# Kernel optimization log

Measured on AMD Instinct MI355X. Metric: run time of the kernel, lower is better.

Reference implementation:

```python
import jax, jax.numpy as jnp
import numpy as np

D_MODEL = 1024
N_HEADS = 16
D_FF = 4096
D_K = D_MODEL // N_HEADS


def _ln(x, g, b, eps=1e-5):
    mu = jnp.mean(x, axis=-1, keepdims=True)
    var = jnp.mean(jnp.square(x - mu), axis=-1, keepdims=True)
    return (x - mu) * jax.lax.rsqrt(var + eps) * g + b


def setup_inputs() -> dict:
    key = jax.random.key(0)
    ks = jax.random.split(key, 16)
    s = 0.02
    inp = {
        "x": jax.random.normal(ks[0], (2, 2048, D_MODEL), dtype=jnp.float32),
        "Wq": jax.random.normal(ks[1], (D_MODEL, D_MODEL), dtype=jnp.float32) * s,
        "bq": jnp.zeros((D_MODEL,), jnp.float32),
        "Wk": jax.random.normal(ks[2], (D_MODEL, D_MODEL), dtype=jnp.float32) * s,
        "bk": jnp.zeros((D_MODEL,), jnp.float32),
        "Wv": jax.random.normal(ks[3], (D_MODEL, D_MODEL), dtype=jnp.float32) * s,
        "bv": jnp.zeros((D_MODEL,), jnp.float32),
        "Wo": jax.random.normal(ks[4], (D_MODEL, D_MODEL), dtype=jnp.float32) * s,
        "bo": jnp.zeros((D_MODEL,), jnp.float32),
        "W1": jax.random.normal(ks[5], (D_MODEL, D_FF), dtype=jnp.float32) * s,
        "b1": jnp.zeros((D_FF,), jnp.float32),
        "W2": jax.random.normal(ks[6], (D_FF, D_MODEL), dtype=jnp.float32) * s,
        "b2": jnp.zeros((D_MODEL,), jnp.float32),
        "g1": jnp.ones((D_MODEL,), jnp.float32),
        "be1": jnp.zeros((D_MODEL,), jnp.float32),
        "g2": jnp.ones((D_MODEL,), jnp.float32),
        "be2": jnp.zeros((D_MODEL,), jnp.float32),
    }
    return inp


def reference(x, Wq, bq, Wk, bk, Wv, bv, Wo, bo, W1, b1, W2, b2, g1, be1, g2, be2):
    B, L, D = x.shape
    # QKV projections -> [B, H, L, d_k]
    q = (x @ Wq + bq).reshape(B, L, N_HEADS, D_K).transpose(0, 2, 1, 3)
    k = (x @ Wk + bk).reshape(B, L, N_HEADS, D_K).transpose(0, 2, 1, 3)
    v = (x @ Wv + bv).reshape(B, L, N_HEADS, D_K).transpose(0, 2, 1, 3)
    scores = jnp.einsum("bhqd,bhkd->bhqk", q, k) / jnp.sqrt(jnp.float32(D_K))
    attn = jax.nn.softmax(scores, axis=-1)
    ctx = jnp.einsum("bhqk,bhkd->bhqd", attn, v)
    ctx = ctx.transpose(0, 2, 1, 3).reshape(B, L, D)
    attn_out = ctx @ Wo + bo
    # residual + LN1
    h = _ln(x + attn_out, g1, be1)
    # FFN (exact GELU, matching torch F.gelu default)
    ff = jax.nn.gelu(h @ W1 + b1, approximate=False) @ W2 + b2
    return _ln(h + ff, g2, be2)
```

## Files before the change

### kernel.cpp

```cpp
#include <hip/hip_runtime.h>
#include <cmath>


typedef unsigned short u16;
typedef unsigned int u32;
typedef __attribute__((ext_vector_type(8))) __bf16 bf16x8;
typedef __attribute__((ext_vector_type(4))) float f32x4;

#define MFMA16(a, b, c) __builtin_amdgcn_mfma_f32_16x16x32_bf16(a, b, c, 0, 0, 0)

__device__ __forceinline__ u16 f2bf(float f) {
  u32 u = __builtin_bit_cast(u32, f);
  u += 0x7fffu + ((u >> 16) & 1u);
  return (u16)(u >> 16);
}

__device__ __forceinline__ u32 packtrunc(float lo, float hi) {
#if __has_builtin(__builtin_amdgcn_perm)
  return __builtin_amdgcn_perm(__builtin_bit_cast(u32, hi),
                               __builtin_bit_cast(u32, lo), 0x07060302u);
#else
  return (__builtin_bit_cast(u32, lo) >> 16) |
         (__builtin_bit_cast(u32, hi) & 0xFFFF0000u);
#endif
}

__device__ __forceinline__ bf16x8 ld_frag(const u16* p) {
  return __builtin_bit_cast(bf16x8, *(const uint4*)p);
}

__device__ __forceinline__ float fexp2(float x) {
#if __has_builtin(__builtin_amdgcn_exp2f)
  return __builtin_amdgcn_exp2f(x);
#else
  return exp2f(x);
#endif
}

__device__ __forceinline__ void gload16(const u16* g, u16* l) {
  __builtin_amdgcn_global_load_lds(
      (const __attribute__((address_space(1))) void*)g,
      (__attribute__((address_space(3))) void*)l, 16, 0, 0);
}

#define WAITVL(N) asm volatile("s_waitcnt vmcnt(" #N ") lgkmcnt(0)" ::: "memory")
#define BAR() do { __builtin_amdgcn_s_barrier(); asm volatile("" ::: "memory"); } while (0)

__global__ __launch_bounds__(256) void cvt_bf16_k(const float* __restrict__ src,
                                                  u16* __restrict__ dst) {
  int i = (blockIdx.x * 256 + threadIdx.x) * 4;
  float4 v = *(const float4*)(src + i);
  ushort4 o;
  o.x = f2bf(v.x); o.y = f2bf(v.y); o.z = f2bf(v.z); o.w = f2bf(v.w);
  *(ushort4*)(dst + i) = o;
}

__global__ __launch_bounds__(256) void transpose_bf16_k(const float* __restrict__ src,
                                                        u16* __restrict__ dst,
                                                        int R, int C) {
  __shared__ float tile[32][33];
  int tx = threadIdx.x & 31, ty = threadIdx.x >> 5;
  int c0 = blockIdx.x * 32, r0 = blockIdx.y * 32;
#pragma unroll
  for (int i = 0; i < 4; i++)
    tile[ty + 8 * i][tx] = src[(long)(r0 + ty + 8 * i) * C + c0 + tx];
  __syncthreads();
#pragma unroll
  for (int i = 0; i < 4; i++)
    dst[(long)(c0 + ty + 8 * i) * R + r0 + tx] = f2bf(tile[tx][ty + 8 * i]);
}

__global__ __launch_bounds__(256) void transpose4_bf16_k(
    const float* __restrict__ Wq, const float* __restrict__ Wk,
    const float* __restrict__ Wv, const float* __restrict__ Wo,
    u16* __restrict__ wqkvT, u16* __restrict__ woT) {
  const int z = blockIdx.z;
  const float* src = (z == 0) ? Wq : (z == 1) ? Wk : (z == 2) ? Wv : Wo;
  u16* dst = (z < 3) ? (wqkvT + (size_t)z * 1024 * 1024) : woT;
  __shared__ float tile[32][33];
  int tx = threadIdx.x & 31, ty = threadIdx.x >> 5;
  int c0 = blockIdx.x * 32, r0 = blockIdx.y * 32;
#pragma unroll
  for (int i = 0; i < 4; i++)
    tile[ty + 8 * i][tx] = src[(long)(r0 + ty + 8 * i) * 1024 + c0 + tx];
  __syncthreads();
#pragma unroll
  for (int i = 0; i < 4; i++)
    dst[(long)(c0 + ty + 8 * i) * 1024 + r0 + tx] = f2bf(tile[tx][ty + 8 * i]);
}

template <int MODE>
__global__ __launch_bounds__(512, 2) void gemm256_k(
    const u16* __restrict__ A, const u16* __restrict__ BT,
    int N, int lda, int ldb, int Kc,
    const float* __restrict__ bias, float* __restrict__ outF, u16* __restrict__ outB,
    float* __restrict__ p1, float* __restrict__ p2, float* __restrict__ p3,
    u16* __restrict__ qd, u16* __restrict__ kd, u16* __restrict__ vTd,
    const float* __restrict__ bq, const float* __restrict__ bk, const float* __restrict__ bv) {
  __shared__ u16 As[4][256 * 32];
  __shared__ u16 Bs[4][256 * 32];
  const int tid = threadIdx.x;
  const int wave = tid >> 6, lane = tid & 63, quad = lane >> 4, l16 = lane & 15;
  const int wm = wave >> 2, wn = wave & 3;
  const int m0 = blockIdx.y * 256, n0 = blockIdx.x * 256;
  const int kz = blockIdx.z;
  const long kofs = (long)kz * Kc;
  const int KT = Kc >> 5;

  const int srow = lane >> 2;
  const int sseg = (lane & 3) ^ (srow & 3);
  const u16* aS = A + (long)(m0 + wave * 32 + srow) * lda + kofs + sseg * 8;
  const u16* bS = BT + (long)(n0 + wave * 32 + srow) * ldb + kofs + sseg * 8;

  auto stageA = [&](int sb, int s) {
    const u16* p = aS + (long)s * 32;
    gload16(p, &As[sb][wave * 1024]);
    gload16(p + 16 * (long)lda, &As[sb][wave * 1024 + 512]);
  };
  auto stageB = [&](int sb, int s) {
    const u16* p = bS + (long)s * 32;
    gload16(p, &Bs[sb][wave * 1024]);
    gload16(p + 16 * (long)ldb, &Bs[sb][wave * 1024 + 512]);
  };

  int aro[8], bro[4];
#pragma unroll
  for (int mf = 0; mf < 8; mf++) {
    int r = wm * 128 + mf * 16 + l16;
    aro[mf] = r * 32 + ((quad ^ (r & 3)) * 8);
  }
#pragma unroll
  for (int nf = 0; nf < 4; nf++) {
    int r = wn * 64 + nf * 16 + l16;
    bro[nf] = r * 32 + ((quad ^ (r & 3)) * 8);
  }

  f32x4 acc[8][4] = {};

  stageA(0, 0); stageB(0, 0);
  stageA(1, 1); stageB(1, 1);
  stageA(2, 2); stageB(2, 2);

#pragma unroll 1
  for (int t = 0; t < KT; ++t) {
    const int buf = t & 3;
    if (t < KT - 2)      { WAITVL(8); }
    else if (t == KT - 2){ WAITVL(4); }
    else                 { WAITVL(0); }
    BAR();

    bf16x8 af[4], bf4[4];
#pragma unroll
    for (int i = 0; i < 4; i++) af[i] = ld_frag(&As[buf][aro[i]]);
#pragma unroll
    for (int i = 0; i < 4; i++) bf4[i] = ld_frag(&Bs[buf][bro[i]]);
    if (t + 3 < KT) stageA((t + 3) & 3, t + 3);
    BAR();
    __builtin_amdgcn_s_setprio(1);
#pragma unroll
    for (int mf = 0; mf < 4; mf++)
#pragma unroll
      for (int nf = 0; nf < 4; nf++)
        acc[mf][nf] = MFMA16(af[mf], bf4[nf], acc[mf][nf]);
    __builtin_amdgcn_s_setprio(0);

    bf16x8 ag[4];
#pragma unroll
    for (int i = 0; i < 4; i++) ag[i] = ld_frag(&As[buf][aro[4 + i]]);
    if (t + 3 < KT) stageB((t + 3) & 3, t + 3);
    BAR();
    __builtin_amdgcn_s_setprio(1);
#pragma unroll
    for (int mf = 0; mf < 4; mf++)
#pragma unroll
      for (int nf = 0; nf < 4; nf++)
        acc[4 + mf][nf] = MFMA16(ag[mf], bf4[nf], acc[4 + mf][nf]);
    __builtin_amdgcn_s_setprio(0);
  }

  if (MODE == 0) {
    const int nbase = n0 + wn * 64;
    const int mat = nbase >> 10;
    const float* bp = (mat == 0) ? bq : ((mat == 1) ? bk : bv);
    float bb[4];
    int hh0[4], dd0[4];
#pragma unroll
    for (int nf = 0; nf < 4; nf++) {
      int nn = (nbase + nf * 16 + l16) & 1023;
      bb[nf] = bp[nn];
      hh0[nf] = nn >> 6;
      dd0[nf] = nn & 63;
    }
    if (mat < 2) {
#pragma unroll
      for (int mf = 0; mf < 8; mf++) {
#pragma unroll
        for (int r = 0; r < 4; r++) {
          int mr = m0 + wm * 128 + mf * 16 + quad * 4 + r;
          int bI = mr >> 11, ll = mr & 2047;
#pragma unroll
          for (int nf = 0; nf < 4; nf++) {
            float v = acc[mf][nf][r] + bb[nf];
            long idx = ((long)((bI * 16 + hh0[nf]) * 2048 + ll)) * 64 + dd0[nf];
            if (mat == 0) {
              qd[idx] = f2bf(v * 0.18033688011112043f);
            } else {
              kd[idx] = f2bf(v);
            }
          }
        }
      }
    } else {
#pragma unroll
      for (int nf = 0; nf < 4; nf++) {
#pragma unroll
        for (int mf = 0; mf < 8; mf++) {
#pragma unroll
          for (int r = 0; r < 4; r++) {
            int mr = m0 + wm * 128 + mf * 16 + quad * 4 + r;
            int bI = mr >> 11, ll = mr & 2047;
            float v = acc[mf][nf][r] + bb[nf];
            vTd[((long)((bI * 16 + hh0[nf]) * 64 + dd0[nf])) * 2048 + ll] = f2bf(v);
          }
        }
      }
    }
  } else if (MODE == 2) {
    float bb[4];
#pragma unroll
    for (int nf = 0; nf < 4; nf++) bb[nf] = bias[n0 + wn * 64 + nf * 16 + l16];
#pragma unroll
    for (int mf = 0; mf < 8; mf++) {
#pragma unroll
      for (int r = 0; r < 4; r++) {
        int mr = m0 + wm * 128 + mf * 16 + quad * 4 + r;
        u16* orow = outB + (long)mr * N + n0 + wn * 64 + l16;
#pragma unroll
        for (int nf = 0; nf < 4; nf++) {
          float v = acc[mf][nf][r] + bb[nf];
          v = 0.5f * v * (1.0f + erff(v * 0.70710678118654752f));
          orow[nf * 16] = f2bf(v);
        }
      }
    }
  } else {
    float* sl = (kz == 0) ? outF : (kz == 1) ? p1 : (kz == 2) ? p2 : p3;
#pragma unroll
    for (int mf = 0; mf < 8; mf++) {
#pragma unroll
      for (int r = 0; r < 4; r++) {
        int mr = m0 + wm * 128 + mf * 16 + quad * 4 + r;
        float* orow = sl + (long)mr * N + n0 + wn * 64 + l16;
#pragma unroll
        for (int nf = 0; nf < 4; nf++) orow[nf * 16] = acc[mf][nf][r];
      }
    }
  }
}

template <int MODE, int TN>
__global__ __launch_bounds__(256) void gemm_k(
    const u16* __restrict__ A, const u16* __restrict__ BT, int M, int N, int K,
    const float* __restrict__ bias, float* __restrict__ outF, u16* __restrict__ outB,
    u16* __restrict__ qd, u16* __restrict__ kd, u16* __restrict__ vTd,
    const float* __restrict__ bq, const float* __restrict__ bk, const float* __restrict__ bv) {
  constexpr int NT = TN / 32;
  __shared__ u16 As[2][128 * 32];
  __shared__ u16 Bs[2][TN * 32];
  const int tid = threadIdx.x;
  const int wave = tid >> 6, lane = tid & 63, quad = lane >> 4, l16 = lane & 15;
  const int wm = wave >> 1, wn = wave & 1;
  const int m0 = blockIdx.y * 128, n0 = blockIdx.x * TN;

  const int srow = lane >> 2;
  const int sxor = (lane & 3) ^ (srow & 3);
  const u16* aS0 = A + (long)(m0 + wave * 32 + srow) * K + sxor * 8;
  const u16* aS1 = aS0 + 16 * K;
  const u16* bS0 = BT + (long)(n0 + (TN == 128 ? wave * 32 : wave * 16) + srow) * K + sxor * 8;
  const u16* bS1 = bS0 + 16 * K;

  int aoff[4], boff[NT];
#pragma unroll
  for (int t = 0; t < 4; t++) {
    int ra = wm * 64 + t * 16 + l16;
    aoff[t] = ra * 32 + ((quad ^ (l16 & 3)) * 8);
  }
#pragma unroll
  for (int t = 0; t < NT; t++) {
    int rb = wn * (TN / 2) + t * 16 + l16;
    boff[t] = rb * 32 + ((quad ^ (l16 & 3)) * 8);
  }

  auto stage = [&](int buf, int k0) {
    gload16(aS0 + k0, &As[buf][(wave * 2 + 0) * 512]);
    gload16(aS1 + k0, &As[buf][(wave * 2 + 1) * 512]);
    if (TN == 128) {
      gload16(bS0 + k0, &Bs[buf][(wave * 2 + 0) * 512]);
      gload16(bS1 + k0, &Bs[buf][(wave * 2 + 1) * 512]);
    } else {
      gload16(bS0 + k0, &Bs[buf][wave * 512]);
    }
  };

  f32x4 acc[4][NT] = {};

  stage(0, 0);
#pragma unroll 1
  for (int k0 = 0; k0 < K; k0 += 32) {
    const int buf = (k0 >> 5) & 1;
    __syncthreads();
    if (k0 + 32 < K) stage(buf ^ 1, k0 + 32);
    bf16x8 af[4], bfr[NT];
#pragma unroll
    for (int t = 0; t < 4; t++) af[t] = ld_frag(&As[buf][aoff[t]]);
#pragma unroll
    for (int t = 0; t < NT; t++) bfr[t] = ld_frag(&Bs[buf][boff[t]]);
#pragma unroll
    for (int mt = 0; mt < 4; mt++)
#pragma unroll
      for (int nt = 0; nt < NT; nt++)
        acc[mt][nt] = MFMA16(af[mt], bfr[nt], acc[mt][nt]);
  }

  if (MODE == 1) {
    float bb[NT];
#pragma unroll
    for (int nt = 0; nt < NT; nt++) bb[nt] = bias[n0 + wn * (TN / 2) + nt * 16 + l16];
#pragma unroll
    for (int mt = 0; mt < 4; mt++) {
#pragma unroll
      for (int r = 0; r < 4; r++) {
        int mr = m0 + wm * 64 + mt * 16 + quad * 4 + r;
        float* orow = outF + (long)mr * N + n0 + wn * (TN / 2) + l16;
#pragma unroll
        for (int nt = 0; nt < NT; nt++)
          orow[nt * 16] = acc[mt][nt][r] + bb[nt];
      }
    }
  }
}

__global__ __launch_bounds__(256) void attn_k(const u16* __restrict__ qd,
                                              const u16* __restrict__ kd,
                                              const u16* __restrict__ vTd,
                                              float* __restrict__ oP0,
                                              float* __restrict__ oP1,
                                              float* __restrict__ ml0,
                                              float* __restrict__ ml1) {
  __shared__ u16 Ks[2][64 * 64];
  __shared__ u16 Vs[2][64 * 64];
  __shared__ __align__(16) u16 P[4][32][72];
  const int tid = threadIdx.x;
  const int wave = tid >> 6, lane = tid & 63, quad = lane >> 4, l16 = lane & 15;
  const int bh = blockIdx.y;
  const int kz = blockIdx.z;
  const int jbeg = kz * 1024, jend = jbeg + 1024;
  const u16* Q = qd + (long)bh * 2048 * 64;
  const u16* Kp = kd + (long)bh * 2048 * 64;
  const u16* Vt = vTd + (long)bh * 64 * 2048;
  const int qbase = blockIdx.x * 128 + wave * 32;

  bf16x8 qf[2][2];
#pragma unroll
  for (int qs = 0; qs < 2; qs++) {
    qf[qs][0] = ld_frag(Q + (qbase + qs * 16 + l16) * 64 + quad * 8);
    qf[qs][1] = ld_frag(Q + (qbase + qs * 16 + l16) * 64 + 32 + quad * 8);
  }

  f32x4 o[2][4] = {};
  float m[2] = {-1e30f, -1e30f}, l[2] = {0.f, 0.f};

  const int srow = lane >> 3;
  const int sx = (lane & 7) ^ srow;
  const int kr0 = wave * 16 + srow;
  const int kr1 = wave * 16 + 8 + srow;

  const int fs0 = ((0 * 4 + quad) ^ (l16 & 7)) * 8;
  const int fs1 = ((1 * 4 + quad) ^ (l16 & 7)) * 8;

  auto stage = [&](int buf, int j0) {
    gload16(Kp + (long)(j0 + kr0) * 64 + sx * 8, &Ks[buf][(wave * 2 + 0) * 512]);
    gload16(Kp + (long)(j0 + kr1) * 64 + sx * 8, &Ks[buf][(wave * 2 + 1) * 512]);
    gload16(Vt + (long)kr0 * 2048 + j0 + sx * 8, &Vs[buf][(wave * 2 + 0) * 512]);
    gload16(Vt + (long)kr1 * 2048 + j0 + sx * 8, &Vs[buf][(wave * 2 + 1) * 512]);
  };

  stage(0, jbeg);

#pragma unroll 1
  for (int j0 = jbeg; j0 < jend; j0 += 64) {
    const int buf = (j0 >> 6) & 1;
    __syncthreads();
    if (j0 + 64 < jend) stage(buf ^ 1, j0 + 64);

    const u16* kb = &Ks[buf][0];
    f32x4 st[2][4];
#pragma unroll
    for (int f = 0; f < 4; f++) {
      bf16x8 k0 = ld_frag(kb + (f * 16 + l16) * 64 + fs0);
      bf16x8 k1 = ld_frag(kb + (f * 16 + l16) * 64 + fs1);
      f32x4 s0 = {}, s1 = {};
      s0 = MFMA16(k0, qf[0][0], s0); s0 = MFMA16(k1, qf[0][1], s0);
      s1 = MFMA16(k0, qf[1][0], s1); s1 = MFMA16(k1, qf[1][1], s1);
      st[0][f] = s0; st[1][f] = s1;
    }

#pragma unroll
    for (int qs = 0; qs < 2; qs++) {
      float mx = -1e30f;
#pragma unroll
      for (int f = 0; f < 4; f++)
        mx = fmaxf(mx, fmaxf(fmaxf(st[qs][f][0], st[qs][f][1]),
                             fmaxf(st[qs][f][2], st[qs][f][3])));
      mx = fmaxf(mx, __shfl_xor(mx, 16));
      mx = fmaxf(mx, __shfl_xor(mx, 32));
      if (__any(mx > m[qs] + 8.0f)) {
        float mn = fmaxf(m[qs], mx);
        float al = fexp2(m[qs] - mn);
        m[qs] = mn;
        l[qs] *= al;
#pragma unroll
        for (int nt = 0; nt < 4; nt++) {
          o[qs][nt][0] *= al; o[qs][nt][1] *= al;
          o[qs][nt][2] *= al; o[qs][nt][3] *= al;
        }
      }
      float sm = 0.f;
      u16* prow = &P[wave][qs * 16 + l16][0];
#pragma unroll
      for (int f = 0; f < 4; f++) {
        float p0 = fexp2(st[qs][f][0] - m[qs]);
        float p1 = fexp2(st[qs][f][1] - m[qs]);
        float p2 = fexp2(st[qs][f][2] - m[qs]);
        float p3 = fexp2(st[qs][f][3] - m[qs]);
        sm += (p0 + p1) + (p2 + p3);
        uint2 u;
        u.x = packtrunc(p0, p1);
        u.y = packtrunc(p2, p3);
        *(uint2*)(prow + f * 16 + quad * 4) = u;
      }
      sm += __shfl_xor(sm, 16);
      sm += __shfl_xor(sm, 32);
      l[qs] += sm;
    }
    __asm__ volatile("s_waitcnt lgkmcnt(0)" ::: "memory");

    const u16* vb = &Vs[buf][0];
    bf16x8 vf[4][2];
#pragma unroll
    for (int nt = 0; nt < 4; nt++) {
      vf[nt][0] = ld_frag(vb + (nt * 16 + l16) * 64 + fs0);
      vf[nt][1] = ld_frag(vb + (nt * 16 + l16) * 64 + fs1);
    }
#pragma unroll
    for (int qs = 0; qs < 2; qs++) {
      const u16* prow = &P[wave][qs * 16 + l16][0];
#pragma unroll
      for (int kh = 0; kh < 2; kh++) {
        bf16x8 pf = ld_frag(prow + kh * 32 + quad * 8);
#pragma unroll
        for (int nt = 0; nt < 4; nt++)
          o[qs][nt] = MFMA16(vf[nt][kh], pf, o[qs][nt]);
      }
    }
  }

  float* oDst = kz ? oP1 : oP0;
  float* mlDst = kz ? ml1 : ml0;
#pragma unroll
  for (int qs = 0; qs < 2; qs++) {
    const long row = (long)bh * 2048 + qbase + qs * 16 + l16;
#pragma unroll
    for (int nt = 0; nt < 4; nt++)
      *(float4*)(oDst + row * 64 + nt * 16 + quad * 4) =
          *(const float4*)&o[qs][nt];
    if (quad == 0) {
      float2 ml2 = {m[qs], l[qs]};
      *(float2*)(mlDst + row * 2) = ml2;
    }
  }
}

__global__ __launch_bounds__(256) void attn_combine_k(
    const float* __restrict__ o0, const float* __restrict__ o1,
    const float* __restrict__ ml0, const float* __restrict__ ml1,
    u16* __restrict__ ctx) {
  long i = ((long)blockIdx.x * 256 + threadIdx.x) * 4;
  long row = i >> 6;
  int d = (int)(i & 63);
  float2 a0 = *(const float2*)(ml0 + row * 2);
  float2 a1 = *(const float2*)(ml1 + row * 2);
  float M = fmaxf(a0.x, a1.x);
  float w0 = fexp2(a0.x - M), w1 = fexp2(a1.x - M);
  float rinv = 1.0f / (a0.y * w0 + a1.y * w1);
  float4 v0 = *(const float4*)(o0 + i);
  float4 v1 = *(const float4*)(o1 + i);
  int bh = (int)(row >> 11), ll = (int)(row & 2047);
  int bI = bh >> 4, hh = bh & 15;
  ushort4 w;
  w.x = f2bf((v0.x * w0 + v1.x * w1) * rinv);
  w.y = f2bf((v0.y * w0 + v1.y * w1) * rinv);
  w.z = f2bf((v0.z * w0 + v1.z * w1) * rinv);
  w.w = f2bf((v0.w * w0 + v1.w * w1) * rinv);
  *(ushort4*)(ctx + ((long)(bI * 2048 + ll) * 1024) + hh * 64 + d) = w;
}

__global__ __launch_bounds__(256) void ln_k(const float* __restrict__ a,
                                            const float* __restrict__ b,
                                            const float* __restrict__ g,
                                            const float* __restrict__ be,
                                            float* __restrict__ outF,
                                            u16* __restrict__ outB) {
  const int row = blockIdx.x, tid = threadIdx.x;
  const float* pa = a + (long)row * 1024;
  const float* pb = b + (long)row * 1024;
  float v[4], s = 0.f, sq = 0.f;
#pragma unroll
  for (int i = 0; i < 4; i++) {
    int c = i * 256 + tid;
    v[i] = pa[c] + pb[c];
    s += v[i];
    sq += v[i] * v[i];
  }
#pragma unroll
  for (int off = 1; off < 64; off <<= 1) {
    s += __shfl_xor(s, off);
    sq += __shfl_xor(sq, off);
  }
  __shared__ float red[10];
  int wave = tid >> 6, lane = tid & 63;
  if (lane == 0) { red[wave * 2] = s; red[wave * 2 + 1] = sq; }
  __syncthreads();
  if (tid == 0) {
    float S = red[0] + red[2] + red[4] + red[6];
    float Q = red[1] + red[3] + red[5] + red[7];
    float mu = S * (1.0f / 1024.0f);
    float var = Q * (1.0f / 1024.0f) - mu * mu;
    red[8] = mu;
    red[9] = rsqrtf(var + 1e-5f);
  }
  __syncthreads();
  float mu = red[8], rstd = red[9];
#pragma unroll
  for (int i = 0; i < 4; i++) {
    int c = i * 256 + tid;
    float o = (v[i] - mu) * rstd * g[c] + be[c];
    outF[(long)row * 1024 + c] = o;
    if (outB) outB[(long)row * 1024 + c] = f2bf(o);
  }
}

__global__ __launch_bounds__(256) void ln4_k(const float* __restrict__ a,
                                             const float* __restrict__ q0,
                                             const float* __restrict__ q1,
                                             const float* __restrict__ q2,
                                             const float* __restrict__ q3,
                                             const float* __restrict__ bias,
                                             const float* __restrict__ g,
                                             const float* __restrict__ be,
                                             float* __restrict__ outF) {
  const int row = blockIdx.x, tid = threadIdx.x;
  const long base = (long)row * 1024;
  float v[4], s = 0.f, sq = 0.f;
#pragma unroll
  for (int i = 0; i < 4; i++) {
    int c = i * 256 + tid;
    float ff = (q0[base + c] + q1[base + c]) + (q2[base + c] + q3[base + c]) + bias[c];
    v[i] = a[base + c] + ff;
    s += v[i];
    sq += v[i] * v[i];
  }
#pragma unroll
  for (int off = 1; off < 64; off <<= 1) {
    s += __shfl_xor(s, off);
    sq += __shfl_xor(sq, off);
  }
  __shared__ float red[10];
  int wave = tid >> 6, lane = tid & 63;
  if (lane == 0) { red[wave * 2] = s; red[wave * 2 + 1] = sq; }
  __syncthreads();
  if (tid == 0) {
    float S = red[0] + red[2] + red[4] + red[6];
    float Q = red[1] + red[3] + red[5] + red[7];
    float mu = S * (1.0f / 1024.0f);
    float var = Q * (1.0f / 1024.0f) - mu * mu;
    red[8] = mu;
    red[9] = rsqrtf(var + 1e-5f);
  }
  __syncthreads();
  float mu = red[8], rstd = red[9];
#pragma unroll
  for (int i = 0; i < 4; i++) {
    int c = i * 256 + tid;
    outF[base + c] = (v[i] - mu) * rstd * g[c] + be[c];
  }
}

extern "C" void kernel_launch(void* const* d_in, const int* in_sizes, int n_in,
                              void* d_out, int out_size, void* d_ws, size_t ws_size,
                              hipStream_t stream) {
  const float* x  = (const float*)d_in[0];
  const float* Wq = (const float*)d_in[1];  const float* bq = (const float*)d_in[2];
  const float* Wk = (const float*)d_in[3];  const float* bk = (const float*)d_in[4];
  const float* Wv = (const float*)d_in[5];  const float* bv = (const float*)d_in[6];
  const float* Wo = (const float*)d_in[7];  const float* bo = (const float*)d_in[8];
  const float* W1 = (const float*)d_in[9];  const float* b1 = (const float*)d_in[10];
  const float* W2 = (const float*)d_in[11]; const float* b2 = (const float*)d_in[12];
  const float* g1 = (const float*)d_in[13]; const float* be1 = (const float*)d_in[14];
  const float* g2 = (const float*)d_in[15]; const float* be2 = (const float*)d_in[16];

  char* ws = (char*)d_ws;
  size_t off = 0;
  auto alloc = [&](size_t bytes) {
    size_t o = off;
    off += (bytes + 255) & ~(size_t)255;
    return o;
  };
  u16*   xb     = (u16*)(ws + alloc(4096UL * 1024 * 2));
  u16*   wqkvT  = (u16*)(ws + alloc(3072UL * 1024 * 2));
  u16*   woT    = (u16*)(ws + alloc(1024UL * 1024 * 2));
  u16*   w1T    = (u16*)(ws + alloc(4096UL * 1024 * 2));
  u16*   w2T    = (u16*)(ws + alloc(1024UL * 4096 * 2));
  u16*   qb     = (u16*)(ws + alloc(32UL * 2048 * 64 * 2));
  u16*   kb     = (u16*)(ws + alloc(32UL * 2048 * 64 * 2));
  u16*   vTb    = (u16*)(ws + alloc(32UL * 64 * 2048 * 2));
  u16*   ctx    = (u16*)(ws + alloc(4096UL * 1024 * 2));
  float* attnO  = (float*)(ws + alloc(4096UL * 1024 * 4));
  float* h      = (float*)(ws + alloc(4096UL * 1024 * 4));
  u16*   hb     = (u16*)(ws + alloc(4096UL * 1024 * 2));
  u16*   ff1    = (u16*)(ws + alloc(4096UL * 4096 * 2));
  float* ff2    = (float*)(ws + alloc(4096UL * 1024 * 4));
  if (off > ws_size) return;

  float* oPart0 = attnO;
  float* oPart1 = h;
  float* mlP0   = (float*)hb;
  float* mlP1   = (float*)hb + 32 * 2048 * 2;

  float* sl0 = ff2;
  float* sl1 = attnO;
  float* sl2 = (float*)qb;
  float* sl3 = (float*)vTb;

  cvt_bf16_k<<<4096, 256, 0, stream>>>(x, xb);
  transpose4_bf16_k<<<dim3(32, 32, 4), 256, 0, stream>>>(Wq, Wk, Wv, Wo, wqkvT, woT);
  transpose_bf16_k<<<dim3(128, 32), 256, 0, stream>>>(W1, w1T, 1024, 4096);
  transpose_bf16_k<<<dim3(32, 128), 256, 0, stream>>>(W2, w2T, 4096, 1024);

  gemm256_k<0><<<dim3(12, 16), 512, 0, stream>>>(
      xb, wqkvT, 3072, 1024, 1024, 1024,
      nullptr, nullptr, nullptr, nullptr, nullptr, nullptr,
      qb, kb, vTb, bq, bk, bv);
  attn_k<<<dim3(16, 32, 2), 256, 0, stream>>>(qb, kb, vTb,
                                              oPart0, oPart1, mlP0, mlP1);
  attn_combine_k<<<4096, 256, 0, stream>>>(oPart0, oPart1, mlP0, mlP1, ctx);
  gemm_k<1, 64><<<dim3(16, 32), 256, 0, stream>>>(ctx, woT, 4096, 1024, 1024,
                                                  bo, attnO, nullptr,
                                                  nullptr, nullptr, nullptr, nullptr, nullptr, nullptr);
  ln_k<<<4096, 256, 0, stream>>>(x, attnO, g1, be1, h, hb);
  gemm256_k<2><<<dim3(16, 16), 512, 0, stream>>>(
      hb, w1T, 4096, 1024, 1024, 1024,
      b1, nullptr, ff1, nullptr, nullptr, nullptr,
      nullptr, nullptr, nullptr, nullptr, nullptr, nullptr);
  gemm256_k<3><<<dim3(4, 16, 4), 512, 0, stream>>>(
      ff1, w2T, 1024, 4096, 4096, 1024,
      nullptr, sl0, nullptr, sl1, sl2, sl3,
      nullptr, nullptr, nullptr, nullptr, nullptr, nullptr);
  ln4_k<<<4096, 256, 0, stream>>>(h, sl0, sl1, sl2, sl3, b2, g2, be2, (float*)d_out);
}
```

Measured before the change: 399.0 us.

## Use 128x128 QKV GEMM kernel and keep attention P in registers via shuffles

The QKV projection now runs on a dedicated 128x128-tile kernel with a 3-stage LDS pipeline, which gives 768 blocks instead of 192 and so better CU occupancy. In attention, softmax probabilities are no longer written to and read back from an LDS P buffer. They are rearranged across lanes with shuffles into the MFMA B-operand layout, using a permuted V fragment swizzle to match. The V fragment loads move earlier, and attn_k gains a launch bound of three blocks per CU. The risks are the extra shuffle and select cost, register pressure under the new occupancy bound, and the smaller QKV tile giving less data reuse.

```diff
diff --git a/kernel.cpp b/kernel.cpp
--- a/kernel.cpp
+++ b/kernel.cpp
@@ -89,14 +89,124 @@
     dst[(long)(c0 + ty + 8 * i) * 1024 + r0 + tx] = f2bf(tile[tx][ty + 8 * i]);
 }
 
+__global__ __launch_bounds__(256, 3) void gemm128_qkv_k(
+    const u16* __restrict__ A, const u16* __restrict__ BT,
+    u16* __restrict__ qd, u16* __restrict__ kd, u16* __restrict__ vTd,
+    const float* __restrict__ bq, const float* __restrict__ bk,
+    const float* __restrict__ bv) {
+  constexpr int K = 1024, KT = 32;
+  __shared__ u16 As[3][128 * 32];
+  __shared__ u16 Bs[3][128 * 32];
+  const int tid = threadIdx.x;
+  const int wave = tid >> 6, lane = tid & 63, quad = lane >> 4, l16 = lane & 15;
+  const int wm = wave >> 1, wn = wave & 1;
+  const int m0 = blockIdx.y * 128, n0 = blockIdx.x * 128;
+
+  const int srow = lane >> 2;
+  const int sseg = (lane & 3) ^ (srow & 3);
+  const u16* aS = A + (long)(m0 + wave * 32 + srow) * K + sseg * 8;
+  const u16* bS = BT + (long)(n0 + wave * 32 + srow) * K + sseg * 8;
+
+  auto stage = [&](int sb, int s) {
+    const u16* pa = aS + s * 32;
+    gload16(pa, &As[sb][wave * 1024]);
+    gload16(pa + 16 * K, &As[sb][wave * 1024 + 512]);
+    const u16* pb = bS + s * 32;
+    gload16(pb, &Bs[sb][wave * 1024]);
+    gload16(pb + 16 * K, &Bs[sb][wave * 1024 + 512]);
+  };
+
+  int aro[4], bro[4];
+#pragma unroll
+  for (int f = 0; f < 4; f++) {
+    int ra = wm * 64 + f * 16 + l16;
+    aro[f] = ra * 32 + ((quad ^ (ra & 3)) * 8);
+    int rb = wn * 64 + f * 16 + l16;
+    bro[f] = rb * 32 + ((quad ^ (rb & 3)) * 8);
+  }
+
+  f32x4 acc[4][4] = {};
+
+  stage(0, 0);
+  stage(1, 1);
+  int buf = 0;
+#pragma unroll 1
+  for (int t = 0; t < KT; ++t) {
+    if (t < KT - 1) { WAITVL(4); } else { WAITVL(0); }
+    BAR();
+    bf16x8 af[4], bfr[4];
+#pragma unroll
+    for (int i = 0; i < 4; i++) af[i] = ld_frag(&As[buf][aro[i]]);
+#pragma unroll
+    for (int i = 0; i < 4; i++) bfr[i] = ld_frag(&Bs[buf][bro[i]]);
+    if (t + 2 < KT) {
+      int nb = buf + 2; if (nb >= 3) nb -= 3;
+      stage(nb, t + 2);
+    }
+    __builtin_amdgcn_s_setprio(1);
+#pragma unroll
+    for (int mf = 0; mf < 4; mf++)
+#pragma unroll
+      for (int nf = 0; nf < 4; nf++)
+        acc[mf][nf] = MFMA16(af[mf], bfr[nf], acc[mf][nf]);
+    __builtin_amdgcn_s_setprio(0);
+    if (++buf == 3) buf = 0;
+  }
+
+  const int nbase = n0 + wn * 64;
+  const int mat = nbase >> 10;
+  const float* bp = (mat == 0) ? bq : ((mat == 1) ? bk : bv);
+  float bb[4];
+  int hh0[4], dd0[4];
+#pragma unroll
+  for (int nf = 0; nf < 4; nf++) {
+    int nn = (nbase + nf * 16 + l16) & 1023;
+    bb[nf] = bp[nn];
+    hh0[nf] = nn >> 6;
+    dd0[nf] = nn & 63;
+  }
+  if (mat < 2) {
+#pragma unroll
+    for (int mf = 0; mf < 4; mf++) {
+#pragma unroll
+      for (int r = 0; r < 4; r++) {
+        int mr = m0 + wm * 64 + mf * 16 + quad * 4 + r;
+        int bI = mr >> 11, ll = mr & 2047;
+#pragma unroll
+        for (int nf = 0; nf < 4; nf++) {
+          float v = acc[mf][nf][r] + bb[nf];
+          long idx = ((long)((bI * 16 + hh0[nf]) * 2048 + ll)) * 64 + dd0[nf];
+          if (mat == 0) {
+            qd[idx] = f2bf(v * 0.18033688011112043f);
+          } else {
+            kd[idx] = f2bf(v);
+          }
+        }
+      }
+    }
+  } else {
+#pragma unroll
+    for (int nf = 0; nf < 4; nf++) {
+#pragma unroll
+      for (int mf = 0; mf < 4; mf++) {
+#pragma unroll
+        for (int r = 0; r < 4; r++) {
+          int mr = m0 + wm * 64 + mf * 16 + quad * 4 + r;
+          int bI = mr >> 11, ll = mr & 2047;
+          float v = acc[mf][nf][r] + bb[nf];
+          vTd[((long)((bI * 16 + hh0[nf]) * 64 + dd0[nf])) * 2048 + ll] = f2bf(v);
+        }
+      }
+    }
+  }
+}
+
 template <int MODE>
 __global__ __launch_bounds__(512, 2) void gemm256_k(
     const u16* __restrict__ A, const u16* __restrict__ BT,
     int N, int lda, int ldb, int Kc,
     const float* __restrict__ bias, float* __restrict__ outF, u16* __restrict__ outB,
-    float* __restrict__ p1, float* __restrict__ p2, float* __restrict__ p3,
-    u16* __restrict__ qd, u16* __restrict__ kd, u16* __restrict__ vTd,
-    const float* __restrict__ bq, const float* __restrict__ bk, const float* __restrict__ bv) {
+    float* __restrict__ p1, float* __restrict__ p2, float* __restrict__ p3) {
   __shared__ u16 As[4][256 * 32];
   __shared__ u16 Bs[4][256 * 32];
   const int tid = threadIdx.x;
@@ -178,54 +288,7 @@
     __builtin_amdgcn_s_setprio(0);
   }
 
-  if (MODE == 0) {
-    const int nbase = n0 + wn * 64;
-    const int mat = nbase >> 10;
-    const float* bp = (mat == 0) ? bq : ((mat == 1) ? bk : bv);
-    float bb[4];
-    int hh0[4], dd0[4];
-#pragma unroll
-    for (int nf = 0; nf < 4; nf++) {
-      int nn = (nbase + nf * 16 + l16) & 1023;
-      bb[nf] = bp[nn];
-      hh0[nf] = nn >> 6;
-      dd0[nf] = nn & 63;
-    }
-    if (mat < 2) {
-#pragma unroll
-      for (int mf = 0; mf < 8; mf++) {
-#pragma unroll
-        for (int r = 0; r < 4; r++) {
-          int mr = m0 + wm * 128 + mf * 16 + quad * 4 + r;
-          int bI = mr >> 11, ll = mr & 2047;
-#pragma unroll
-          for (int nf = 0; nf < 4; nf++) {
-            float v = acc[mf][nf][r] + bb[nf];
-            long idx = ((long)((bI * 16 + hh0[nf]) * 2048 + ll)) * 64 + dd0[nf];
-            if (mat == 0) {
-              qd[idx] = f2bf(v * 0.18033688011112043f);
-            } else {
-              kd[idx] = f2bf(v);
-            }
-          }
-        }
-      }
-    } else {
-#pragma unroll
-      for (int nf = 0; nf < 4; nf++) {
-#pragma unroll
-        for (int mf = 0; mf < 8; mf++) {
-#pragma unroll
-          for (int r = 0; r < 4; r++) {
-            int mr = m0 + wm * 128 + mf * 16 + quad * 4 + r;
-            int bI = mr >> 11, ll = mr & 2047;
-            float v = acc[mf][nf][r] + bb[nf];
-            vTd[((long)((bI * 16 + hh0[nf]) * 64 + dd0[nf])) * 2048 + ll] = f2bf(v);
-          }
-        }
-      }
-    }
-  } else if (MODE == 2) {
+  if (MODE == 2) {
     float bb[4];
 #pragma unroll
     for (int nf = 0; nf < 4; nf++) bb[nf] = bias[n0 + wn * 64 + nf * 16 + l16];
@@ -261,9 +324,7 @@
 template <int MODE, int TN>
 __global__ __launch_bounds__(256) void gemm_k(
     const u16* __restrict__ A, const u16* __restrict__ BT, int M, int N, int K,
-    const float* __restrict__ bias, float* __restrict__ outF, u16* __restrict__ outB,
-    u16* __restrict__ qd, u16* __restrict__ kd, u16* __restrict__ vTd,
-    const float* __restrict__ bq, const float* __restrict__ bk, const float* __restrict__ bv) {
+    const float* __restrict__ bias, float* __restrict__ outF) {
   constexpr int NT = TN / 32;
   __shared__ u16 As[2][128 * 32];
   __shared__ u16 Bs[2][TN * 32];
@@ -340,16 +401,15 @@
   }
 }
 
-__global__ __launch_bounds__(256) void attn_k(const u16* __restrict__ qd,
-                                              const u16* __restrict__ kd,
-                                              const u16* __restrict__ vTd,
-                                              float* __restrict__ oP0,
-                                              float* __restrict__ oP1,
-                                              float* __restrict__ ml0,
-                                              float* __restrict__ ml1) {
+__global__ __launch_bounds__(256, 3) void attn_k(const u16* __restrict__ qd,
+                                                 const u16* __restrict__ kd,
+                                                 const u16* __restrict__ vTd,
+                                                 float* __restrict__ oP0,
+                                                 float* __restrict__ oP1,
+                                                 float* __restrict__ ml0,
+                                                 float* __restrict__ ml1) {
   __shared__ u16 Ks[2][64 * 64];
   __shared__ u16 Vs[2][64 * 64];
-  __shared__ __align__(16) u16 P[4][32][72];
   const int tid = threadIdx.x;
   const int wave = tid >> 6, lane = tid & 63, quad = lane >> 4, l16 = lane & 15;
   const int bh = blockIdx.y;
@@ -377,6 +437,9 @@
 
   const int fs0 = ((0 * 4 + quad) ^ (l16 & 7)) * 8;
   const int fs1 = ((1 * 4 + quad) ^ (l16 & 7)) * 8;
+  const int sV = ((quad & 1) << 1) | (quad >> 1);
+  const int fv0 = ((0 * 4 + sV) ^ (l16 & 7)) * 8;
+  const int fv1 = ((1 * 4 + sV) ^ (l16 & 7)) * 8;
 
   auto stage = [&](int buf, int j0) {
     gload16(Kp + (long)(j0 + kr0) * 64 + sx * 8, &Ks[buf][(wave * 2 + 0) * 512]);
@@ -403,6 +466,14 @@
       s0 = MFMA16(k0, qf[0][0], s0); s0 = MFMA16(k1, qf[0][1], s0);
       s1 = MFMA16(k0, qf[1][0], s1); s1 = MFMA16(k1, qf[1][1], s1);
       st[0][f] = s0; st[1][f] = s1;
+    }
+
+    const u16* vb = &Vs[buf][0];
+    bf16x8 vf[4][2];
+#pragma unroll
+    for (int nt = 0; nt < 4; nt++) {
+      vf[nt][0] = ld_frag(vb + (nt * 16 + l16) * 64 + fv0);
+      vf[nt][1] = ld_frag(vb + (nt * 16 + l16) * 64 + fv1);
     }
 
 #pragma unroll
@@ -426,7 +497,7 @@
         }
       }
       float sm = 0.f;
-      u16* prow = &P[wave][qs * 16 + l16][0];
+      u32 wp[4][2];
 #pragma unroll
       for (int f = 0; f < 4; f++) {
         float p0 = fexp2(st[qs][f][0] - m[qs]);
@@ -434,30 +505,26 @@
         float p2 = fexp2(st[qs][f][2] - m[qs]);
         float p3 = fexp2(st[qs][f][3] - m[qs]);
         sm += (p0 + p1) + (p2 + p3);
-        uint2 u;
-        u.x = packtrunc(p0, p1);
-        u.y = packtrunc(p2, p3);
-        *(uint2*)(prow + f * 16 + quad * 4) = u;
+        wp[f][0] = packtrunc(p0, p1);
+        wp[f][1] = packtrunc(p2, p3);
       }
       sm += __shfl_xor(sm, 16);
       sm += __shfl_xor(sm, 32);
       l[qs] += sm;
-    }
-    __asm__ volatile("s_waitcnt lgkmcnt(0)" ::: "memory");
-
-    const u16* vb = &Vs[buf][0];
-    bf16x8 vf[4][2];
-#pragma unroll
-    for (int nt = 0; nt < 4; nt++) {
-      vf[nt][0] = ld_frag(vb + (nt * 16 + l16) * 64 + fs0);
-      vf[nt][1] = ld_frag(vb + (nt * 16 + l16) * 64 + fs1);
-    }
-#pragma unroll
-    for (int qs = 0; qs < 2; qs++) {
-      const u16* prow = &P[wave][qs * 16 + l16][0];
+
 #pragma unroll
       for (int kh = 0; kh < 2; kh++) {
-        bf16x8 pf = ld_frag(prow + kh * 32 + quad * 8);
+        const int flo = kh * 2, fhi = flo + 1;
+        u32 tx0 = (quad & 1) ? wp[flo][0] : wp[fhi][0];
+        u32 tx1 = (quad & 1) ? wp[flo][1] : wp[fhi][1];
+        u32 rx0 = __shfl_xor(tx0, 16);
+        u32 rx1 = __shfl_xor(tx1, 16);
+        uint4 fw;
+        fw.x = (quad & 1) ? rx0 : wp[flo][0];
+        fw.y = (quad & 1) ? rx1 : wp[flo][1];
+        fw.z = (quad & 1) ? wp[fhi][0] : rx0;
+        fw.w = (quad & 1) ? wp[fhi][1] : rx1;
+        bf16x8 pf = __builtin_bit_cast(bf16x8, fw);
 #pragma unroll
         for (int nt = 0; nt < 4; nt++)
           o[qs][nt] = MFMA16(vf[nt][kh], pf, o[qs][nt]);
@@ -550,15 +617,15 @@
   }
 }
 
-__global__ __launch_bounds__(256) void ln4_k(const float* __restrict__ a,
-                                             const float* __restrict__ q0,
-                                             const float* __restrict__ q1,
-                                             const float* __restrict__ q2,
-                                             const float* __restrict__ q3,
-                                             const float* __restrict__ bias,
-                                             const float* __restrict__ g,
-                                             const float* __restrict__ be,
-                                             float* __restrict__ outF) {
+__global__ __launch_bounds__(256) void ln4b_k(const float* __restrict__ a,
+                                              const float* __restrict__ q0,
+                                              const float* __restrict__ q1,
+                                              const float* __restrict__ q2,
+                                              const float* __restrict__ q3,
+                                              const float* __restrict__ bias,
+                                              const float* __restrict__ g,
+                                              const float* __restrict__ be,
+                                              float* __restrict__ outF) {
   const int row = blockIdx.x, tid = threadIdx.x;
   const long base = (long)row * 1024;
   float v[4], s = 0.f, sq = 0.f;
@@ -647,24 +714,20 @@
   transpose_bf16_k<<<dim3(128, 32), 256, 0, stream>>>(W1, w1T, 1024, 4096);
   transpose_bf16_k<<<dim3(32, 128), 256, 0, stream>>>(W2, w2T, 4096, 1024);
 
-  gemm256_k<0><<<dim3(12, 16), 512, 0, stream>>>(
-      xb, wqkvT, 3072, 1024, 1024, 1024,
-      nullptr, nullptr, nullptr, nullptr, nullptr, nullptr,
-      qb, kb, vTb, bq, bk, bv);
+  gemm128_qkv_k<<<dim3(24, 32), 256, 0, stream>>>(xb, wqkvT, qb, kb, vTb,
+                                                  bq, bk, bv);
   attn_k<<<dim3(16, 32, 2), 256, 0, stream>>>(qb, kb, vTb,
                                               oPart0, oPart1, mlP0, mlP1);
   attn_combine_k<<<4096, 256, 0, stream>>>(oPart0, oPart1, mlP0, mlP1, ctx);
   gemm_k<1, 64><<<dim3(16, 32), 256, 0, stream>>>(ctx, woT, 4096, 1024, 1024,
-                                                  bo, attnO, nullptr,
-                                                  nullptr, nullptr, nullptr, nullptr, nullptr, nullptr);
+                                                  bo, attnO);
   ln_k<<<4096, 256, 0, stream>>>(x, attnO, g1, be1, h, hb);
   gemm256_k<2><<<dim3(16, 16), 512, 0, stream>>>(
       hb, w1T, 4096, 1024, 1024, 1024,
-      b1, nullptr, ff1, nullptr, nullptr, nullptr,
-      nullptr, nullptr, nullptr, nullptr, nullptr, nullptr);
+      b1, nullptr, ff1, nullptr, nullptr, nullptr);
   gemm256_k<3><<<dim3(4, 16, 4), 512, 0, stream>>>(
       ff1, w2T, 1024, 4096, 4096, 1024,
-      nullptr, sl0, nullptr, sl1, sl2, sl3,
-      nullptr, nullptr, nullptr, nullptr, nullptr, nullptr);
-  ln4_k<<<4096, 256, 0, stream>>>(h, sl0, sl1, sl2, sl3, b2, g2, be2, (float*)d_out);
-}
+      nullptr, sl0, nullptr, sl1, sl2, sl3);
+  ln4b_k<<<4096, 256, 0, stream>>>(h, sl0, sl1, sl2, sl3, b2, g2, be2,
+                                   (float*)d_out);
+}
```

New measurement: 400.6 us. No clear change (+0.4%).
